# Kernel tuning notes

Hardware: AMD Instinct MI355X
Metric: run time of the kernel (lower is better)

## Reference

```python
import jax, jax.numpy as jnp
import numpy as np

N_NODES = 100000

def gcn_conv(x, W, b, row, col, n):
    # PyG GCNConv: linear transform, then D^-1/2 A_hat D^-1/2 aggregation (+bias).
    xw = x @ W                                            # [N, out]
    deg = jax.ops.segment_sum(jnp.ones_like(col, dtype=xw.dtype), col, num_segments=n)
    dinv = jnp.where(deg > 0, jax.lax.rsqrt(jnp.maximum(deg, 1e-12)), 0.0)
    norm = dinv[row] * dinv[col]                          # [E]
    msgs = xw[row] * norm[:, None]                        # gather + scale
    out = jax.ops.segment_sum(msgs, col, num_segments=n)  # scatter-add
    return out + b


def setup_inputs() -> dict:
    key = jax.random.key(0)
    k = jax.random.split(key, 9)
    n, e = N_NODES, 1600000
    d_in, d_h, d_out = 128, 64, 40
    def glorot(kk, fi, fo):
        s = jnp.sqrt(6.0 / (fi + fo))
        return jax.random.uniform(kk, (fi, fo), jnp.float32, -s, s)
    return {
        "x": jax.random.normal(k[0], (n, d_in), jnp.float32),
        "edge_index": jax.random.randint(k[1], (2, e), 0, n, jnp.int64),
        "W1": glorot(k[2], d_in, d_h), "b1": jnp.zeros((d_h,), jnp.float32),
        "W2": glorot(k[3], d_h, d_h),  "b2": jnp.zeros((d_h,), jnp.float32),
        "W3": glorot(k[4], d_h, d_out), "b3": jnp.zeros((d_out,), jnp.float32),
    }


def reference(x, edge_index, W1, b1, W2, b2, W3, b3):
    n = x.shape[0]
    loops = jnp.arange(n, dtype=edge_index.dtype)
    row = jnp.concatenate([edge_index[0], loops])  # self-loops added, as in GCNConv
    col = jnp.concatenate([edge_index[1], loops])
    h = jax.nn.relu(gcn_conv(x, W1, b1, row, col, n))
    h = jax.nn.relu(gcn_conv(h, W2, b2, row, col, n))
    return gcn_conv(h, W3, b3, row, col, n)
```

## Files before the change

### kernel.cpp

```cpp
#include <hip/hip_runtime.h>
#include <hip/hip_fp16.h>

constexpr int TPB = 256;
constexpr int SH = 9;
constexpr int BD = 1 << SH;
constexpr int CHUNK = 4096;

typedef _Float16 half8 __attribute__((ext_vector_type(8)));
typedef float float4v __attribute__((ext_vector_type(4)));

__device__ __forceinline__ int wave_incl_scan(int x, int lane) {
#pragma unroll
  for (int d = 1; d < 64; d <<= 1) {
    int y = __shfl_up(x, d);
    if (lane >= d) x += y;
  }
  return x;
}


__global__ void bin_kernel(const int* __restrict__ row, const int* __restrict__ col,
                           int* __restrict__ bcur, int2* __restrict__ binned,
                           int e, int nb, int cap) {
  __shared__ int h[512];
  __shared__ int base[512];
  for (int i = threadIdx.x; i < nb; i += TPB) h[i] = 0;
  __syncthreads();
  int cb = blockIdx.x * CHUNK;
  int lim = min(cb + CHUNK, e);
  for (int i = cb + threadIdx.x; i < lim; i += TPB)
    atomicAdd(&h[col[i] >> SH], 1);
  __syncthreads();
  for (int i = threadIdx.x; i < nb; i += TPB) {
    int c = h[i];
    base[i] = c ? (i * cap + atomicAdd(&bcur[i], c)) : 0;
    h[i] = 0;
  }
  __syncthreads();
  for (int i = cb + threadIdx.x; i < lim; i += TPB) {
    int c = col[i];
    int b = c >> SH;
    int p = base[b] + atomicAdd(&h[b], 1);
    binned[p] = make_int2(row[i], c);
  }
}

__global__ __launch_bounds__(512) void count_place_kernel(
    const int2* __restrict__ binned, const int* __restrict__ bcnt, int cap,
    int2* __restrict__ offs2, float* __restrict__ dinv, int* __restrict__ csr, int n) {
  __shared__ int cnt[BD];
  __shared__ int wsum[8];
  int t = threadIdx.x, lane = t & 63, wv = t >> 6;
  int b = blockIdx.x;
  int c0 = b << SH;
  int ndst = min(BD, n - c0);
  cnt[t] = 0;
  __syncthreads();
  int beg = b * cap;
  int end = beg + bcnt[b];
  for (int i = beg + t; i < end; i += 512)
    atomicAdd(&cnt[binned[i].y - c0], 1);
  __syncthreads();
  int v = cnt[t];
  int ps = wave_incl_scan(v, lane);
  if (lane == 63) wsum[wv] = ps;
  __syncthreads();
  int woff = 0;
#pragma unroll
  for (int w = 0; w < 8; w++) woff += (w < wv) ? wsum[w] : 0;
  int ex = woff + ps - v;
  if (t < ndst) {
    offs2[c0 + t] = make_int2(beg + ex, beg + ex + v);
    dinv[c0 + t] = rsqrtf(1.0f + (float)v);
  }
  __syncthreads();
  cnt[t] = beg + ex;
  __syncthreads();
  for (int i = beg + t; i < end; i += 512) {
    int2 rc = binned[i];
    int p = atomicAdd(&cnt[rc.y - c0], 1);
    csr[p] = rc.x;
  }
}


template <int K, int M, int CT, int KT>
__global__ void pack_w_kernel(const float* __restrict__ W, _Float16* __restrict__ P) {
  int idx = blockIdx.x * TPB + threadIdx.x;
  if (idx >= CT * KT * 64 * 8) return;
  int j = idx & 7;
  int lane = (idx >> 3) & 63;
  int f = idx >> 9;
  int kt = f % KT, ct = f / KT;
  int c = ct * 16 + (lane & 15);
  int k = kt * 32 + (lane >> 4) * 8 + j;
  float v = (c < M) ? W[k * M + c] : 0.f;
  P[idx] = (_Float16)v;
}

template <int K, int M, int CT>
__global__ __launch_bounds__(256) void gemm_mfma_f32in(const float* __restrict__ x,
                                                       const _Float16* __restrict__ PW,
                                                       _Float16* __restrict__ out, int n) {
  constexpr int KT = K / 32;
  int lane = threadIdx.x & 63, wv = threadIdx.x >> 6;
  int m = lane & 15, q = lane >> 4;
  int row0w = blockIdx.x * 64 + wv * 16;
  int arow = row0w + m;
  int ar = arow < n ? arow : n - 1;
  const half8* pw = (const half8*)PW;

  float4v acc[CT];
#pragma unroll
  for (int ct = 0; ct < CT; ct++) acc[ct] = (float4v){0.f, 0.f, 0.f, 0.f};

#pragma unroll
  for (int kt = 0; kt < KT; kt++) {
    const float* xp = x + (size_t)ar * K + kt * 32 + q * 8;
    float4 x0 = *(const float4*)xp;
    float4 x1 = *(const float4*)(xp + 4);
    half8 a;
    a[0] = (_Float16)x0.x; a[1] = (_Float16)x0.y;
    a[2] = (_Float16)x0.z; a[3] = (_Float16)x0.w;
    a[4] = (_Float16)x1.x; a[5] = (_Float16)x1.y;
    a[6] = (_Float16)x1.z; a[7] = (_Float16)x1.w;
#pragma unroll
    for (int ct = 0; ct < CT; ct++) {
      half8 b = pw[(ct * KT + kt) * 64 + lane];
      acc[ct] = __builtin_amdgcn_mfma_f32_16x16x32_f16(a, b, acc[ct], 0, 0, 0);
    }
  }
  int r0 = row0w + q * 4;
#pragma unroll
  for (int ct = 0; ct < CT; ct++) {
    int c = ct * 16 + m;
    if (c < M) {
#pragma unroll
      for (int reg = 0; reg < 4; reg++) {
        int r = r0 + reg;
        if (r < n) out[(size_t)r * M + c] = (_Float16)acc[ct][reg];
      }
    }
  }
}

template <int K, int M, int CT>
__global__ __launch_bounds__(256) void gemm_mfma_f16in(const _Float16* __restrict__ x,
                                                       const _Float16* __restrict__ PW,
                                                       _Float16* __restrict__ out, int n) {
  constexpr int KT = K / 32;
  int lane = threadIdx.x & 63, wv = threadIdx.x >> 6;
  int m = lane & 15, q = lane >> 4;
  int row0w = blockIdx.x * 64 + wv * 16;
  int arow = row0w + m;
  int ar = arow < n ? arow : n - 1;
  const half8* pw = (const half8*)PW;

  float4v acc[CT];
#pragma unroll
  for (int ct = 0; ct < CT; ct++) acc[ct] = (float4v){0.f, 0.f, 0.f, 0.f};

#pragma unroll
  for (int kt = 0; kt < KT; kt++) {
    half8 a = *(const half8*)(x + (size_t)ar * K + kt * 32 + q * 8);
#pragma unroll
    for (int ct = 0; ct < CT; ct++) {
      half8 b = pw[(ct * KT + kt) * 64 + lane];
      acc[ct] = __builtin_amdgcn_mfma_f32_16x16x32_f16(a, b, acc[ct], 0, 0, 0);
    }
  }
  int r0 = row0w + q * 4;
#pragma unroll
  for (int ct = 0; ct < CT; ct++) {
    int c = ct * 16 + m;
    if (c < M) {
#pragma unroll
      for (int reg = 0; reg < 4; reg++) {
        int r = r0 + reg;
        if (r < n) out[(size_t)r * M + c] = (_Float16)acc[ct][reg];
      }
    }
  }
}

template <int K, int M, int CT>
__global__ __launch_bounds__(256) void gemm_mfma_f16in_f32out(
    const _Float16* __restrict__ x, const _Float16* __restrict__ PW,
    const float* __restrict__ bias, float* __restrict__ out, int n) {
  constexpr int KT = K / 32;
  int lane = threadIdx.x & 63, wv = threadIdx.x >> 6;
  int m = lane & 15, q = lane >> 4;
  int row0w = blockIdx.x * 64 + wv * 16;
  int arow = row0w + m;
  int ar = arow < n ? arow : n - 1;
  const half8* pw = (const half8*)PW;

  float4v acc[CT];
#pragma unroll
  for (int ct = 0; ct < CT; ct++) acc[ct] = (float4v){0.f, 0.f, 0.f, 0.f};

#pragma unroll
  for (int kt = 0; kt < KT; kt++) {
    half8 a = *(const half8*)(x + (size_t)ar * K + kt * 32 + q * 8);
#pragma unroll
    for (int ct = 0; ct < CT; ct++) {
      half8 b = pw[(ct * KT + kt) * 64 + lane];
      acc[ct] = __builtin_amdgcn_mfma_f32_16x16x32_f16(a, b, acc[ct], 0, 0, 0);
    }
  }
  int r0 = row0w + q * 4;
#pragma unroll
  for (int ct = 0; ct < CT; ct++) {
    int c = ct * 16 + m;
    if (c < M) {
      float bb = bias[c];
#pragma unroll
      for (int reg = 0; reg < 4; reg++) {
        int r = r0 + reg;
        if (r < n) out[(size_t)r * M + c] = acc[ct][reg] + bb;
      }
    }
  }
}


__device__ __forceinline__ void h4_fma(uint2 u, float nrm, float4& acc) {
  __half2 h0 = *(__half2*)&u.x, h1 = *(__half2*)&u.y;
  float2 f0 = __half22float2(h0), f1 = __half22float2(h1);
  acc.x = fmaf(f0.x, nrm, acc.x);
  acc.y = fmaf(f0.y, nrm, acc.y);
  acc.z = fmaf(f1.x, nrm, acc.z);
  acc.w = fmaf(f1.y, nrm, acc.w);
}

template <bool RELU_BIAS>
__global__ __launch_bounds__(256) void agg64_kernel(
    const uint2* __restrict__ xw2, const float* __restrict__ dinv,
    const int* __restrict__ csr, const int2* __restrict__ offs2,
    const float* __restrict__ bias, uint2* __restrict__ out2, int n) {
  int lane = threadIdx.x & 63, wv = threadIdx.x >> 6;
  int slot = lane >> 4, fl = lane & 15;
  int sb = slot << 4;
  int i = blockIdx.x * 16 + wv * 4 + slot;
  bool valid = i < n;
  int ic = valid ? i : n - 1;
  int2 oe = offs2[ic];
  int beg = oe.x;
  int end = valid ? oe.y : beg;
  float di = dinv[ic];
  float4 acc = {0.f, 0.f, 0.f, 0.f};
  h4_fma(xw2[(size_t)ic * 16 + fl], di, acc);

  for (int b = beg; b < end; b += 16) {
    int idx = b + fl;
    int rr = 0;
    float dd = 0.f;
    if (idx < end) {
      rr = csr[idx];
      dd = dinv[rr];
    }
    int cnt = end - b;
    uint2 u[16];
#pragma unroll
    for (int j = 0; j < 16; j++) {
      if (j < cnt) {
        int r = __shfl(rr, sb + j);
        u[j] = xw2[(size_t)r * 16 + fl];
      }
    }
#pragma unroll
    for (int j = 0; j < 16; j++) {
      if (j < cnt) {
        float nrm = __shfl(dd, sb + j);
        h4_fma(u[j], nrm, acc);
      }
    }
  }

  if (valid) {
    float4 o;
    if (RELU_BIAS) {
      const float4* b4 = (const float4*)bias;
      float4 bb = b4[fl];
      o.x = fmaxf(acc.x * di + bb.x, 0.f);
      o.y = fmaxf(acc.y * di + bb.y, 0.f);
      o.z = fmaxf(acc.z * di + bb.z, 0.f);
      o.w = fmaxf(acc.w * di + bb.w, 0.f);
    } else {
      o.x = acc.x * di; o.y = acc.y * di;
      o.z = acc.z * di; o.w = acc.w * di;
    }
    __half2 h0 = __float22half2_rn(make_float2(o.x, o.y));
    __half2 h1 = __float22half2_rn(make_float2(o.z, o.w));
    uint2 u;
    u.x = *(unsigned*)&h0;
    u.y = *(unsigned*)&h1;
    out2[(size_t)i * 16 + fl] = u;
  }
}


extern "C" void kernel_launch(void* const* d_in, const int* in_sizes, int n_in,
                              void* d_out, int out_size, void* d_ws, size_t ws_size,
                              hipStream_t stream) {
  const float* x  = (const float*)d_in[0];
  const int*   ei = (const int*)d_in[1];
  const float* W1 = (const float*)d_in[2];
  const float* b1 = (const float*)d_in[3];
  const float* W2 = (const float*)d_in[4];
  const float* b2 = (const float*)d_in[5];
  const float* W3 = (const float*)d_in[6];
  const float* b3 = (const float*)d_in[7];

  int n = in_sizes[0] / 128;
  int e = in_sizes[1] / 2;
  const int* rowA = ei;
  const int* colA = ei + e;

  int nb = (n + BD - 1) >> SH;
  int meanb = e / nb;
  int cap = meanb + (meanb / 4 > 1024 ? meanb / 4 : 1024);
  int nch = (e + CHUNK - 1) / CHUNK;

  size_t off = 0;
  auto alloc = [&](size_t bytes) {
    void* p = (char*)d_ws + off;
    off += (bytes + 255) & ~(size_t)255;
    return p;
  };
  __half* bufA  = (__half*)alloc((size_t)n * 64 * 4);
  __half* bufB  = (__half*)alloc((size_t)n * 64 * 4);
  int2*  offs2  = (int2*)alloc((size_t)n * 8);
  float* dinv   = (float*)alloc((size_t)n * 4);
  int*   csr    = (int*)alloc((size_t)nb * cap * 4);
  int*   bcur   = (int*)alloc(512 * 4);
  _Float16* PW1 = (_Float16*)alloc(4 * 4 * 64 * 8 * 2);
  _Float16* PW2 = (_Float16*)alloc(4 * 2 * 64 * 8 * 2);
  _Float16* PW3 = (_Float16*)alloc(3 * 2 * 64 * 8 * 2);
  int2*  binned = (int2*)bufA;
  (void)ws_size; (void)n_in; (void)out_size;

  hipMemsetAsync(bcur, 0, (size_t)nb * 4, stream);
  bin_kernel<<<nch, TPB, 0, stream>>>(rowA, colA, bcur, binned, e, nb, cap);
  count_place_kernel<<<nb, 512, 0, stream>>>(binned, bcur, cap, offs2, dinv, csr, n);

  pack_w_kernel<128, 64, 4, 4><<<(4 * 4 * 512 + TPB - 1) / TPB, TPB, 0, stream>>>(W1, PW1);
  pack_w_kernel<64, 64, 4, 2><<<(4 * 2 * 512 + TPB - 1) / TPB, TPB, 0, stream>>>(W2, PW2);
  pack_w_kernel<64, 40, 3, 2><<<(3 * 2 * 512 + TPB - 1) / TPB, TPB, 0, stream>>>(W3, PW3);

  int gmf = (n + 63) / 64;
  int gagg = (n + 15) / 16;
  gemm_mfma_f32in<128, 64, 4><<<gmf, TPB, 0, stream>>>(x, PW1, (_Float16*)bufA, n);
  agg64_kernel<true><<<gagg, TPB, 0, stream>>>((const uint2*)bufA, dinv, csr, offs2,
                                               b1, (uint2*)bufB, n);
  gemm_mfma_f16in<64, 64, 4><<<gmf, TPB, 0, stream>>>((const _Float16*)bufB, PW2,
                                                      (_Float16*)bufA, n);
  agg64_kernel<true><<<gagg, TPB, 0, stream>>>((const uint2*)bufA, dinv, csr, offs2,
                                               b2, (uint2*)bufB, n);
  agg64_kernel<false><<<gagg, TPB, 0, stream>>>((const uint2*)bufB, dinv, csr, offs2,
                                                nullptr, (uint2*)bufA, n);
  gemm_mfma_f16in_f32out<64, 40, 3><<<gmf, TPB, 0, stream>>>((const _Float16*)bufA, PW3,
                                                             b3, (float*)d_out, n);
}
```

Baseline: 273.2 us.

## Prescale rows by dinv in GEMM epilogues and widen aggregation to 16-byte loads

The source-side normalization dinv[row] moves into the GEMM epilogues, and into the layer-2 aggregation output for the final layer. This removes the per-edge dinv gather and FMA from the aggregation loop, leaving plain half-to-float adds. The aggregation kernel now uses 8 lanes per node with uint4 (8-half) loads instead of 16 lanes with uint2, so each wave handles twice as many nodes. The three weight-pack kernels and the bcur memset are merged into one launch. Pre-scaling in fp16 before accumulation slightly changes rounding.

Result: slower. 281.2 us (+2.9%).

```diff
diff --git a/kernel.cpp b/kernel.cpp
--- a/kernel.cpp
+++ b/kernel.cpp
@@ -85,8 +85,8 @@
 
 
 template <int K, int M, int CT, int KT>
-__global__ void pack_w_kernel(const float* __restrict__ W, _Float16* __restrict__ P) {
-  int idx = blockIdx.x * TPB + threadIdx.x;
+__device__ __forceinline__ void pack_one(const float* __restrict__ W,
+                                         _Float16* __restrict__ P, int idx) {
   if (idx >= CT * KT * 64 * 8) return;
   int j = idx & 7;
   int lane = (idx >> 3) & 63;
@@ -98,9 +98,28 @@
   P[idx] = (_Float16)v;
 }
 
+__global__ __launch_bounds__(256) void pack_all_kernel(
+    const float* __restrict__ W1, const float* __restrict__ W2,
+    const float* __restrict__ W3, _Float16* __restrict__ P1,
+    _Float16* __restrict__ P2, _Float16* __restrict__ P3, int* __restrict__ bcur) {
+  int blk = blockIdx.x, t = threadIdx.x;
+  if (blk < 32) {
+    pack_one<128, 64, 4, 4>(W1, P1, blk * 256 + t);
+  } else if (blk < 48) {
+    pack_one<64, 64, 4, 2>(W2, P2, (blk - 32) * 256 + t);
+  } else if (blk < 60) {
+    pack_one<64, 40, 3, 2>(W3, P3, (blk - 48) * 256 + t);
+  } else {
+    bcur[t] = 0;
+    bcur[t + 256] = 0;
+  }
+}
+
+
 template <int K, int M, int CT>
 __global__ __launch_bounds__(256) void gemm_mfma_f32in(const float* __restrict__ x,
                                                        const _Float16* __restrict__ PW,
+                                                       const float* __restrict__ dinv,
                                                        _Float16* __restrict__ out, int n) {
   constexpr int KT = K / 32;
   int lane = threadIdx.x & 63, wv = threadIdx.x >> 6;
@@ -131,6 +150,9 @@
     }
   }
   int r0 = row0w + q * 4;
+  float dv[4];
+#pragma unroll
+  for (int reg = 0; reg < 4; reg++) dv[reg] = (r0 + reg < n) ? dinv[r0 + reg] : 0.f;
 #pragma unroll
   for (int ct = 0; ct < CT; ct++) {
     int c = ct * 16 + m;
@@ -138,7 +160,7 @@
 #pragma unroll
       for (int reg = 0; reg < 4; reg++) {
         int r = r0 + reg;
-        if (r < n) out[(size_t)r * M + c] = (_Float16)acc[ct][reg];
+        if (r < n) out[(size_t)r * M + c] = (_Float16)(acc[ct][reg] * dv[reg]);
       }
     }
   }
@@ -147,6 +169,7 @@
 template <int K, int M, int CT>
 __global__ __launch_bounds__(256) void gemm_mfma_f16in(const _Float16* __restrict__ x,
                                                        const _Float16* __restrict__ PW,
+                                                       const float* __restrict__ dinv,
                                                        _Float16* __restrict__ out, int n) {
   constexpr int KT = K / 32;
   int lane = threadIdx.x & 63, wv = threadIdx.x >> 6;
@@ -170,6 +193,9 @@
     }
   }
   int r0 = row0w + q * 4;
+  float dv[4];
+#pragma unroll
+  for (int reg = 0; reg < 4; reg++) dv[reg] = (r0 + reg < n) ? dinv[r0 + reg] : 0.f;
 #pragma unroll
   for (int ct = 0; ct < CT; ct++) {
     int c = ct * 16 + m;
@@ -177,7 +203,7 @@
 #pragma unroll
       for (int reg = 0; reg < 4; reg++) {
         int r = r0 + reg;
-        if (r < n) out[(size_t)r * M + c] = (_Float16)acc[ct][reg];
+        if (r < n) out[(size_t)r * M + c] = (_Float16)(acc[ct][reg] * dv[reg]);
       }
     }
   }
@@ -224,78 +250,83 @@
 }
 
 
-__device__ __forceinline__ void h4_fma(uint2 u, float nrm, float4& acc) {
+__device__ __forceinline__ void h8_add(uint4 u, float* acc) {
   __half2 h0 = *(__half2*)&u.x, h1 = *(__half2*)&u.y;
+  __half2 h2 = *(__half2*)&u.z, h3 = *(__half2*)&u.w;
   float2 f0 = __half22float2(h0), f1 = __half22float2(h1);
-  acc.x = fmaf(f0.x, nrm, acc.x);
-  acc.y = fmaf(f0.y, nrm, acc.y);
-  acc.z = fmaf(f1.x, nrm, acc.z);
-  acc.w = fmaf(f1.y, nrm, acc.w);
-}
-
-template <bool RELU_BIAS>
-__global__ __launch_bounds__(256) void agg64_kernel(
-    const uint2* __restrict__ xw2, const float* __restrict__ dinv,
+  float2 f2 = __half22float2(h2), f3 = __half22float2(h3);
+  acc[0] += f0.x; acc[1] += f0.y; acc[2] += f1.x; acc[3] += f1.y;
+  acc[4] += f2.x; acc[5] += f2.y; acc[6] += f3.x; acc[7] += f3.y;
+}
+
+template <int MODE>
+__global__ __launch_bounds__(256) void agg_kernel(
+    const uint4* __restrict__ xw4, const float* __restrict__ dinv,
     const int* __restrict__ csr, const int2* __restrict__ offs2,
-    const float* __restrict__ bias, uint2* __restrict__ out2, int n) {
+    const float* __restrict__ bias, uint4* __restrict__ out4, int n) {
   int lane = threadIdx.x & 63, wv = threadIdx.x >> 6;
-  int slot = lane >> 4, fl = lane & 15;
-  int sb = slot << 4;
-  int i = blockIdx.x * 16 + wv * 4 + slot;
+  int slot = lane >> 3, fl = lane & 7;
+  int sb = slot << 3;
+  int i = blockIdx.x * 32 + wv * 8 + slot;
   bool valid = i < n;
   int ic = valid ? i : n - 1;
   int2 oe = offs2[ic];
   int beg = oe.x;
   int end = valid ? oe.y : beg;
   float di = dinv[ic];
-  float4 acc = {0.f, 0.f, 0.f, 0.f};
-  h4_fma(xw2[(size_t)ic * 16 + fl], di, acc);
-
-  for (int b = beg; b < end; b += 16) {
+  float acc[8] = {0.f, 0.f, 0.f, 0.f, 0.f, 0.f, 0.f, 0.f};
+  h8_add(xw4[(size_t)ic * 8 + fl], acc);
+
+  for (int b = beg; b < end; b += 8) {
     int idx = b + fl;
     int rr = 0;
-    float dd = 0.f;
-    if (idx < end) {
-      rr = csr[idx];
-      dd = dinv[rr];
-    }
+    if (idx < end) rr = csr[idx];
     int cnt = end - b;
-    uint2 u[16];
-#pragma unroll
-    for (int j = 0; j < 16; j++) {
+    uint4 u[8];
+#pragma unroll
+    for (int j = 0; j < 8; j++) {
       if (j < cnt) {
         int r = __shfl(rr, sb + j);
-        u[j] = xw2[(size_t)r * 16 + fl];
-      }
-    }
-#pragma unroll
-    for (int j = 0; j < 16; j++) {
-      if (j < cnt) {
-        float nrm = __shfl(dd, sb + j);
-        h4_fma(u[j], nrm, acc);
-      }
+        u[j] = xw4[(size_t)r * 8 + fl];
+      }
+    }
+#pragma unroll
+    for (int j = 0; j < 8; j++) {
+      if (j < cnt) h8_add(u[j], acc);
     }
   }
 
   if (valid) {
-    float4 o;
-    if (RELU_BIAS) {
+    float o[8];
+    if (MODE < 2) {
       const float4* b4 = (const float4*)bias;
-      float4 bb = b4[fl];
-      o.x = fmaxf(acc.x * di + bb.x, 0.f);
-      o.y = fmaxf(acc.y * di + bb.y, 0.f);
-      o.z = fmaxf(acc.z * di + bb.z, 0.f);
-      o.w = fmaxf(acc.w * di + bb.w, 0.f);
+      float4 ba = b4[fl * 2], bb = b4[fl * 2 + 1];
+      o[0] = fmaxf(acc[0] * di + ba.x, 0.f);
+      o[1] = fmaxf(acc[1] * di + ba.y, 0.f);
+      o[2] = fmaxf(acc[2] * di + ba.z, 0.f);
+      o[3] = fmaxf(acc[3] * di + ba.w, 0.f);
+      o[4] = fmaxf(acc[4] * di + bb.x, 0.f);
+      o[5] = fmaxf(acc[5] * di + bb.y, 0.f);
+      o[6] = fmaxf(acc[6] * di + bb.z, 0.f);
+      o[7] = fmaxf(acc[7] * di + bb.w, 0.f);
+      if (MODE == 1) {
+#pragma unroll
+        for (int k = 0; k < 8; k++) o[k] *= di;
+      }
     } else {
-      o.x = acc.x * di; o.y = acc.y * di;
-      o.z = acc.z * di; o.w = acc.w * di;
-    }
-    __half2 h0 = __float22half2_rn(make_float2(o.x, o.y));
-    __half2 h1 = __float22half2_rn(make_float2(o.z, o.w));
-    uint2 u;
+#pragma unroll
+      for (int k = 0; k < 8; k++) o[k] = acc[k] * di;
+    }
+    __half2 h0 = __float22half2_rn(make_float2(o[0], o[1]));
+    __half2 h1 = __float22half2_rn(make_float2(o[2], o[3]));
+    __half2 h2 = __float22half2_rn(make_float2(o[4], o[5]));
+    __half2 h3 = __float22half2_rn(make_float2(o[6], o[7]));
+    uint4 u;
     u.x = *(unsigned*)&h0;
     u.y = *(unsigned*)&h1;
-    out2[(size_t)i * 16 + fl] = u;
+    u.z = *(unsigned*)&h2;
+    u.w = *(unsigned*)&h3;
+    out4[(size_t)i * 8 + fl] = u;
   }
 }
 
@@ -340,25 +371,21 @@
   int2*  binned = (int2*)bufA;
   (void)ws_size; (void)n_in; (void)out_size;
 
-  hipMemsetAsync(bcur, 0, (size_t)nb * 4, stream);
+  pack_all_kernel<<<61, TPB, 0, stream>>>(W1, W2, W3, PW1, PW2, PW3, bcur);
   bin_kernel<<<nch, TPB, 0, stream>>>(rowA, colA, bcur, binned, e, nb, cap);
   count_place_kernel<<<nb, 512, 0, stream>>>(binned, bcur, cap, offs2, dinv, csr, n);
 
-  pack_w_kernel<128, 64, 4, 4><<<(4 * 4 * 512 + TPB - 1) / TPB, TPB, 0, stream>>>(W1, PW1);
-  pack_w_kernel<64, 64, 4, 2><<<(4 * 2 * 512 + TPB - 1) / TPB, TPB, 0, stream>>>(W2, PW2);
-  pack_w_kernel<64, 40, 3, 2><<<(3 * 2 * 512 + TPB - 1) / TPB, TPB, 0, stream>>>(W3, PW3);
-
   int gmf = (n + 63) / 64;
-  int gagg = (n + 15) / 16;
-  gemm_mfma_f32in<128, 64, 4><<<gmf, TPB, 0, stream>>>(x, PW1, (_Float16*)bufA, n);
-  agg64_kernel<true><<<gagg, TPB, 0, stream>>>((const uint2*)bufA, dinv, csr, offs2,
-                                               b1, (uint2*)bufB, n);
-  gemm_mfma_f16in<64, 64, 4><<<gmf, TPB, 0, stream>>>((const _Float16*)bufB, PW2,
+  int gagg = (n + 31) / 32;
+  gemm_mfma_f32in<128, 64, 4><<<gmf, TPB, 0, stream>>>(x, PW1, dinv, (_Float16*)bufA, n);
+  agg_kernel<0><<<gagg, TPB, 0, stream>>>((const uint4*)bufA, dinv, csr, offs2,
+                                          b1, (uint4*)bufB, n);
+  gemm_mfma_f16in<64, 64, 4><<<gmf, TPB, 0, stream>>>((const _Float16*)bufB, PW2, dinv,
                                                       (_Float16*)bufA, n);
-  agg64_kernel<true><<<gagg, TPB, 0, stream>>>((const uint2*)bufA, dinv, csr, offs2,
-                                               b2, (uint2*)bufB, n);
-  agg64_kernel<false><<<gagg, TPB, 0, stream>>>((const uint2*)bufB, dinv, csr, offs2,
-                                                nullptr, (uint2*)bufA, n);
+  agg_kernel<1><<<gagg, TPB, 0, stream>>>((const uint4*)bufA, dinv, csr, offs2,
+                                          b2, (uint4*)bufB, n);
+  agg_kernel<2><<<gagg, TPB, 0, stream>>>((const uint4*)bufB, dinv, csr, offs2,
+                                          nullptr, (uint4*)bufA, n);
   gemm_mfma_f16in_f32out<64, 40, 3><<<gmf, TPB, 0, stream>>>((const _Float16*)bufA, PW3,
                                                              b3, (float*)d_out, n);
 }
```
